# Kernel tuning notes

Measured on AMD Instinct MI355X. Metric: run time of the kernel, lower is better.

Reference implementation:

```python
import jax, jax.numpy as jnp
import numpy as np

# ---- static configuration matching init_kwargs ----
SEG = 2                 # segment_size hard-coded in the module
MUL0, MUL1 = 256, 128   # irreps = 256x0e + 128x1o
G = MUL1 // SEG         # 64 groups of 2x1o
INV_DIM = MUL0 + 3 * G  # 448 scalars (0e) after concat with channel_mix
N_IRREPS = INV_DIM + MUL1 + G + 3 * G  # 832 total irreps after regroup
N_NODES = 32768
EPS = 1e-6
_ISQ2 = 1.0 / np.sqrt(2.0)
_ISQ3 = 1.0 / np.sqrt(3.0)
_ISQ6 = 1.0 / np.sqrt(6.0)


def _cg_l2(a, b):
    """CG contraction 1 x 1 -> 2: project a_i b_j onto the 5 orthonormal
    symmetric-traceless basis matrices. a, b: [..., 3] -> [..., 5]."""
    ax, ay, az = a[..., 0], a[..., 1], a[..., 2]
    bx, by, bz = b[..., 0], b[..., 1], b[..., 2]
    return jnp.stack([
        (ax * by + ay * bx) * _ISQ2,
        (ax * bz + az * bx) * _ISQ2,
        (ay * bz + az * by) * _ISQ2,
        (ax * bx - ay * by) * _ISQ2,
        (2 * az * bz - ax * bx - ay * by) * _ISQ6,
    ], axis=-1)


def setup_inputs() -> dict:
    key = jax.random.key(0)
    k = jax.random.split(key, 5)
    return {
        "x":   jax.random.normal(k[0], (N_NODES, MUL0 + 3 * MUL1), dtype=jnp.float32),
        "W1":  jax.random.normal(k[1], (INV_DIM, INV_DIM),   dtype=jnp.float32),
        "W2":  jax.random.normal(k[2], (INV_DIM, N_IRREPS),  dtype=jnp.float32),
        "Wl0": jax.random.normal(k[3], (INV_DIM, MUL0),      dtype=jnp.float32),
        "Wl1": jax.random.normal(k[4], (MUL1, MUL1),         dtype=jnp.float32),
    }


def reference(x, W1, W2, Wl0, Wl1):
    N = x.shape[0]
    dt = x.dtype
    s = x[:, :MUL0]                       # [N, 256]  0e features
    v = x[:, MUL0:].reshape(N, MUL1, 3)   # [N, 128, 3]  1o features

    # ---- segmented tensor_square: groups of 2x1o -> 3x0e + 1x1e + 3x2e ----
    vg = v.reshape(N, G, SEG, 3)
    a, b = vg[:, :, 0], vg[:, :, 1]
    sq2 = jnp.sqrt(jnp.asarray(2.0, dt))
    # 0e: symmetric pairs (0,0), (0,1)*sqrt2, (1,1); CG = delta_ij/sqrt3
    t0 = jnp.stack([(a * a).sum(-1), sq2 * (a * b).sum(-1), (b * b).sum(-1)], -1) * _ISQ3  # [N,G,3]
    # 1e: antisymmetric pair (0,1); CG = eps/sqrt2, pair factor sqrt2 -> plain cross
    t1 = jnp.cross(a, b)                                                                   # [N,G,3]
    # 2e: symmetric pairs
    t2 = jnp.stack([_cg_l2(a, a), sq2 * _cg_l2(a, b), _cg_l2(b, b)], 2)                    # [N,G,3,5]

    # ---- concatenate + regroup (axis_to_mul folds group axis into mul) ----
    s_all = jnp.concatenate([s, t0.reshape(N, 3 * G)], -1)  # [N,448]  448x0e
    v1o = v                                                 # [N,128,3] 128x1o
    v1e = t1                                                # [N,64,3]   64x1e
    v2e = t2.reshape(N, 3 * G, 5)                           # [N,192,5] 192x2e

    # ---- gating MLP on invariants: [448 -> 448 (silu) -> 832] ----
    inv_fan = jnp.sqrt(jnp.asarray(INV_DIM, dt))
    h = jax.nn.silu(s_all @ W1 / inv_fan)
    gates = h @ W2 / inv_fan                                # [N, 832] one scalar per irrep
    g0, g1o, g1e, g2e = jnp.split(gates, [INV_DIM, INV_DIM + MUL1, INV_DIM + MUL1 + G], -1)
    s_all = s_all * g0
    v1o = v1o * g1o[..., None]
    # (v1e * g1e, v2e * g2e are dropped by the Linear below -> omitted, output identical)
    del v1e, v2e, g1e, g2e

    # ---- e3nn Linear to output irreps 256x0e + 128x1o (1e, 2e have no output) ----
    o0 = s_all @ Wl0 / inv_fan                                                   # [N,256]
    o1 = jnp.einsum('nmi,mk->nki', v1o, Wl1) / jnp.sqrt(jnp.asarray(MUL1, dt))   # [N,128,3]

    # ---- equivariant layer norm ----
    mu = o0.mean(-1, keepdims=True)
    var = ((o0 - mu) ** 2).mean(-1, keepdims=True)
    o0 = (o0 - mu) * jax.lax.rsqrt(var + EPS)
    rms = jnp.sqrt((o1 ** 2).mean((-2, -1), keepdims=True) + EPS)
    o1 = o1 / rms

    return jnp.concatenate([o0, o1.reshape(N, 3 * MUL1)], -1)  # [N, 640]
```

## Files before the change

kernel.cpp:

```cpp
#include <hip/hip_runtime.h>
#include <math.h>


typedef float floatx4 __attribute__((ext_vector_type(4)));
typedef __bf16 bf16x8 __attribute__((ext_vector_type(8)));

__device__ __forceinline__ unsigned short f2bf(float f) {
    union { float f; unsigned u; } v; v.f = f;
    unsigned r = v.u + 0x7FFFu + ((v.u >> 16) & 1u);
    return (unsigned short)(r >> 16);
}
__device__ __forceinline__ float bf2f(unsigned short u) {
    union { unsigned u; float f; } v; v.u = ((unsigned)u) << 16; return v.f;
}

__global__ __launch_bounds__(256) void wcast_kernel(
    const float* __restrict__ W1, const float* __restrict__ W2,
    const float* __restrict__ Wl0, const float* __restrict__ Wl1,
    unsigned short* __restrict__ W1T, unsigned short* __restrict__ W2T,
    unsigned short* __restrict__ Wl0T, unsigned short* __restrict__ Wl1T)
{
    int idx = blockIdx.x * 256 + threadIdx.x;
    if (idx < 200704) {
        int j = idx / 448, k = idx - j * 448;
        W1T[idx] = f2bf(W1[k * 448 + j]);
    } else if (idx < 200704 + 258048) {
        int r = idx - 200704;
        int j = r / 448, k = r - j * 448;
        W2T[r] = f2bf(W2[k * 832 + j]);
    } else if (idx < 200704 + 258048 + 114688) {
        int r = idx - (200704 + 258048);
        int j = r / 448, k = r - j * 448;
        Wl0T[r] = f2bf(Wl0[k * 256 + j]);
    } else if (idx < 200704 + 258048 + 114688 + 16384) {
        int r = idx - (200704 + 258048 + 114688);
        int j = r / 128, m = r - j * 128;
        Wl1T[r] = f2bf(Wl1[m * 128 + j]);
    }
}

template<int MT, int NT>
__device__ __forceinline__ void gemm_ktiles(
    const unsigned short* __restrict__ Bt, const int ldb, const int kTot, const int colBase,
    const unsigned short* __restrict__ Albs, const int ldsA, const int rowBase,
    unsigned short* __restrict__ Bs,
    const int tid, const int l15, const int quad, const int wn,
    floatx4 (&acc)[MT][NT])
{
    constexpr int NU = NT * 256;
    for (int k0 = 0; k0 < kTot; k0 += 32) {
        __syncthreads();
        #pragma unroll
        for (int u0 = 0; u0 < NU; u0 += 512) {
            int u = u0 + tid;
            if (u0 + 512 <= NU || u < NU) {
                int col = u >> 2, part = u & 3;
                *(uint4*)&Bs[col * 40 + part * 8] =
                    *(const uint4*)(Bt + (colBase + col) * ldb + k0 + part * 8);
            }
        }
        __syncthreads();
        bf16x8 af[MT];
        #pragma unroll
        for (int mt = 0; mt < MT; ++mt)
            af[mt] = *(const bf16x8*)&Albs[(rowBase + mt * 16 + l15) * ldsA + k0 + quad * 8];
        #pragma unroll
        for (int j = 0; j < NT; ++j) {
            bf16x8 bfv = *(const bf16x8*)&Bs[((wn + 4 * j) * 16 + l15) * 40 + quad * 8];
            #pragma unroll
            for (int mt = 0; mt < MT; ++mt)
                acc[mt][j] = __builtin_amdgcn_mfma_f32_16x16x32_bf16(af[mt], bfv, acc[mt][j], 0, 0, 0);
        }
    }
}

__global__ __launch_bounds__(512, 2) void fused_kernel(
    const float* __restrict__ x,
    const unsigned short* __restrict__ W1T,
    const unsigned short* __restrict__ W2T,
    const unsigned short* __restrict__ Wl0T,
    const unsigned short* __restrict__ Wl1T,
    float* __restrict__ out)
{
    __shared__ unsigned short sa[64][472];
    __shared__ unsigned short hb[64][472];
    __shared__ unsigned short BsG1[17920];
    __shared__ float red[832];

    const int tid  = threadIdx.x;
    const int lane = tid & 63;
    const int l15  = lane & 15;
    const int quad = lane >> 4;
    const int w    = tid >> 6;
    const int wm   = w >> 2;
    const int wn   = w & 3;
    const int n0   = blockIdx.x * 64;

    const float s1 = 0.047245559f;
    const float s2 = 0.088388348f;

    {
        const int r = tid >> 3, sub = tid & 7;
        const float* xr = x + (size_t)(n0 + r) * 640;
        #pragma unroll
        for (int i = 0; i < 8; ++i) {
            int c4 = i * 8 + sub;
            float4 f = *(const float4*)(xr + c4 * 4);
            uint2 p;
            p.x = (unsigned)f2bf(f.x) | ((unsigned)f2bf(f.y) << 16);
            p.y = (unsigned)f2bf(f.z) | ((unsigned)f2bf(f.w) << 16);
            *(uint2*)&sa[r][c4 * 4] = p;
        }
        const float* xv = xr + 256;
        #pragma unroll
        for (int i = 0; i < 8; ++i) {
            int g = i * 8 + sub;
            const float2* vg = (const float2*)(xv + 6 * g);
            float2 p0 = vg[0], p1 = vg[1], p2 = vg[2];
            float ax = p0.x, ay = p0.y, az = p1.x;
            float bx = p1.y, by = p2.x, bz = p2.y;
            float aa = ax*ax + ay*ay + az*az;
            float ab = ax*bx + ay*by + az*bz;
            float bb = bx*bx + by*by + bz*bz;
            const float ISQ3 = 0.57735026918962576f;
            const float SQ2  = 1.41421356237309505f;
            sa[r][256 + 3*g]     = f2bf(aa * ISQ3);
            sa[r][256 + 3*g + 1] = f2bf(SQ2 * ab * ISQ3);
            sa[r][256 + 3*g + 2] = f2bf(bb * ISQ3);
        }
    }

    {
        floatx4 acc[2][7] = {};
        gemm_ktiles<2,7>(W1T, 448, 448, 0, &sa[0][0], 472, wm*32, BsG1, tid, l15, quad, wn, acc);
        #pragma unroll
        for (int j = 0; j < 7; ++j) {
            const int col = (wn + 4*j) * 16 + l15;
            #pragma unroll
            for (int mt = 0; mt < 2; ++mt)
                #pragma unroll
                for (int r = 0; r < 4; ++r) {
                    float v = acc[mt][j][r] * s1;
                    v = v / (1.f + __expf(-v));
                    hb[wm*32 + mt*16 + quad*4 + r][col] = f2bf(v);
                }
        }
    }

    {
        floatx4 acc1[2][5] = {};
        floatx4 acc2[2][4] = {};
        gemm_ktiles<2,5>(W2T, 448, 448, 0,   &hb[0][0], 472, wm*32, BsG1, tid, l15, quad, wn, acc1);
        gemm_ktiles<2,4>(W2T, 448, 448, 320, &hb[0][0], 472, wm*32, BsG1, tid, l15, quad, wn, acc2);
        __syncthreads();
        unsigned short* g1p = BsG1;
        #pragma unroll
        for (int j = 0; j < 5; ++j) {
            const int col = (wn + 4*j) * 16 + l15;
            #pragma unroll
            for (int mt = 0; mt < 2; ++mt)
                #pragma unroll
                for (int r = 0; r < 4; ++r) {
                    const int row = wm*32 + mt*16 + quad*4 + r;
                    hb[row][col] = f2bf(bf2f(sa[row][col]) * (acc1[mt][j][r] * s1));
                }
        }
        #pragma unroll
        for (int j = 0; j < 4; ++j) {
            const int colb = 320 + (wn + 4*j) * 16;
            if (colb < 448) {
                const int col = colb + l15;
                #pragma unroll
                for (int mt = 0; mt < 2; ++mt)
                    #pragma unroll
                    for (int r = 0; r < 4; ++r) {
                        const int row = wm*32 + mt*16 + quad*4 + r;
                        hb[row][col] = f2bf(bf2f(sa[row][col]) * (acc2[mt][j][r] * s1));
                    }
            } else {
                const int m = colb - 448 + l15;
                #pragma unroll
                for (int mt = 0; mt < 2; ++mt)
                    #pragma unroll
                    for (int r = 0; r < 4; ++r) {
                        const int row = wm*32 + mt*16 + quad*4 + r;
                        g1p[row * 128 + m] = f2bf(acc2[mt][j][r] * s1);
                    }
            }
        }
        __syncthreads();
    }

    {
        unsigned short* wmp = &sa[0][0];
        const unsigned short* g1p = BsG1;
        #pragma unroll
        for (int e0 = 0; e0 < 6144; e0 += 512) {
            int e4 = e0 + tid;
            int rl = e4 / 96;
            int c4 = (e4 - rl * 96) * 4;
            float4 xv = *(const float4*)(x + (size_t)(n0 + rl) * 640 + 256 + c4);
            float vv[4] = {xv.x, xv.y, xv.z, xv.w};
            #pragma unroll
            for (int d = 0; d < 4; ++d) {
                int rem = c4 + d;
                int m = rem / 3;
                int i = rem - 3 * m;
                wmp[(rl * 3 + i) * 136 + m] = f2bf(vv[d] * bf2f(g1p[rl * 128 + m]));
            }
        }
        __syncthreads();
    }

    {
        floatx4 acc[2][4] = {};
        gemm_ktiles<2,4>(Wl0T, 448, 448, 0, &hb[0][0], 472, wm*32, BsG1, tid, l15, quad, wn, acc);
        #pragma unroll
        for (int mt = 0; mt < 2; ++mt)
            #pragma unroll
            for (int r = 0; r < 4; ++r) {
                float sv = 0.f, sq = 0.f;
                #pragma unroll
                for (int j = 0; j < 4; ++j) {
                    float v = acc[mt][j][r] * s1;
                    sv += v; sq += v * v;
                }
                #pragma unroll
                for (int off = 1; off <= 8; off <<= 1) {
                    sv += __shfl_xor(sv, off);
                    sq += __shfl_xor(sq, off);
                }
                if (l15 == 0) {
                    const int row = wm*32 + mt*16 + quad*4 + r;
                    red[row * 8 + wn * 2]     = sv;
                    red[row * 8 + wn * 2 + 1] = sq;
                }
            }
        __syncthreads();
        #pragma unroll
        for (int mt = 0; mt < 2; ++mt)
            #pragma unroll
            for (int r = 0; r < 4; ++r) {
                const int row = wm*32 + mt*16 + quad*4 + r;
                float ts = red[row*8+0] + red[row*8+2] + red[row*8+4] + red[row*8+6];
                float tq = red[row*8+1] + red[row*8+3] + red[row*8+5] + red[row*8+7];
                float mu  = ts * (1.f/256.f);
                float var = tq * (1.f/256.f) - mu * mu;
                float rln = rsqrtf(var + 1e-6f);
                float* orow = out + (size_t)(n0 + row) * 640;
                #pragma unroll
                for (int j = 0; j < 4; ++j)
                    orow[(wn + 4*j)*16 + l15] = (acc[mt][j][r] * s1 - mu) * rln;
            }
    }

    {
        floatx4 acc[6][2] = {};
        gemm_ktiles<6,2>(Wl1T, 128, 128, 0, &sa[0][0] , 136, wm*96, BsG1, tid, l15, quad, wn, acc);
        #pragma unroll
        for (int mt = 0; mt < 6; ++mt)
            #pragma unroll
            for (int r = 0; r < 4; ++r) {
                float q = 0.f;
                #pragma unroll
                for (int j = 0; j < 2; ++j) {
                    float v = acc[mt][j][r] * s2;
                    q += v * v;
                }
                #pragma unroll
                for (int off = 1; off <= 8; off <<= 1) q += __shfl_xor(q, off);
                if (l15 == 0) {
                    const int row = wm*96 + mt*16 + quad*4 + r;
                    red[row * 4 + wn] = q;
                }
            }
        __syncthreads();
        if (tid < 64) {
            float s = 0.f;
            #pragma unroll
            for (int rr = 0; rr < 3; ++rr)
                #pragma unroll
                for (int w2 = 0; w2 < 4; ++w2)
                    s += red[(tid*3 + rr) * 4 + w2];
            red[768 + tid] = rsqrtf(s * (1.f/384.f) + 1e-6f);
        }
        __syncthreads();
        #pragma unroll
        for (int mt = 0; mt < 6; ++mt)
            #pragma unroll
            for (int r = 0; r < 4; ++r) {
                const int row = wm*96 + mt*16 + quad*4 + r;
                const int nl  = row / 3;
                const int i   = row - 3 * nl;
                const float rms = red[768 + nl];
                float* op = out + (size_t)(n0 + nl) * 640 + 256 + i;
                #pragma unroll
                for (int j = 0; j < 2; ++j)
                    op[3 * ((wn + 4*j)*16 + l15)] = acc[mt][j][r] * s2 * rms;
            }
    }
}

extern "C" void kernel_launch(void* const* d_in, const int* in_sizes, int n_in,
                              void* d_out, int out_size, void* d_ws, size_t ws_size,
                              hipStream_t stream) {
    const float* x   = (const float*)d_in[0];
    const float* W1  = (const float*)d_in[1];
    const float* W2  = (const float*)d_in[2];
    const float* Wl0 = (const float*)d_in[3];
    const float* Wl1 = (const float*)d_in[4];
    float* out = (float*)d_out;
    char* ws = (char*)d_ws;

    unsigned short* W1T  = (unsigned short*)(ws + 0);
    unsigned short* W2T  = (unsigned short*)(ws + 401408);
    unsigned short* Wl0T = (unsigned short*)(ws + 917504);
    unsigned short* Wl1T = (unsigned short*)(ws + 1146880);

    wcast_kernel<<<dim3(2304), dim3(256), 0, stream>>>(W1, W2, Wl0, Wl1, W1T, W2T, Wl0T, Wl1T);
    fused_kernel<<<dim3(512), dim3(512), 0, stream>>>(x, W1T, W2T, Wl0T, Wl1T, out);
}
```

Baseline: 283.2 us.

## Pre-swizzle weights into MFMA fragment order and stream B directly from global

The weight-cast kernel now writes each weight matrix in a layout where every lane's 8-element bf16 B fragment is contiguous per 16-column tile and 32-wide k-chunk. The GEMM loop then loads B fragments straight from global/L2 into registers, with no LDS staging and no per-k-tile __syncthreads. The two W2 GEMM passes are merged into one with 9 column tiles, and explicit barriers are added between stages. This removes LDS traffic and barrier stalls, at the cost of relying on L2 and cache latency for every B load, with no explicit prefetch.

```diff
diff --git a/kernel.cpp b/kernel.cpp
--- a/kernel.cpp
+++ b/kernel.cpp
@@ -17,56 +17,60 @@
 __global__ __launch_bounds__(256) void wcast_kernel(
     const float* __restrict__ W1, const float* __restrict__ W2,
     const float* __restrict__ Wl0, const float* __restrict__ Wl1,
-    unsigned short* __restrict__ W1T, unsigned short* __restrict__ W2T,
-    unsigned short* __restrict__ Wl0T, unsigned short* __restrict__ Wl1T)
+    unsigned short* __restrict__ W1F, unsigned short* __restrict__ W2F,
+    unsigned short* __restrict__ Wl0F, unsigned short* __restrict__ Wl1F)
 {
     int idx = blockIdx.x * 256 + threadIdx.x;
     if (idx < 200704) {
-        int j = idx / 448, k = idx - j * 448;
-        W1T[idx] = f2bf(W1[k * 448 + j]);
-    } else if (idx < 200704 + 258048) {
+        int e = idx & 7, lane = (idx >> 3) & 63, r2 = idx >> 9;
+        int kc = r2 % 14, t = r2 / 14;
+        int col = t * 16 + (lane & 15);
+        int k   = kc * 32 + (lane >> 4) * 8 + e;
+        W1F[idx] = f2bf(W1[k * 448 + col]);
+    } else if (idx < 458752) {
         int r = idx - 200704;
-        int j = r / 448, k = r - j * 448;
-        W2T[r] = f2bf(W2[k * 832 + j]);
-    } else if (idx < 200704 + 258048 + 114688) {
-        int r = idx - (200704 + 258048);
-        int j = r / 448, k = r - j * 448;
-        Wl0T[r] = f2bf(Wl0[k * 256 + j]);
-    } else if (idx < 200704 + 258048 + 114688 + 16384) {
-        int r = idx - (200704 + 258048 + 114688);
-        int j = r / 128, m = r - j * 128;
-        Wl1T[r] = f2bf(Wl1[m * 128 + j]);
-    }
-}
-
-template<int MT, int NT>
-__device__ __forceinline__ void gemm_ktiles(
-    const unsigned short* __restrict__ Bt, const int ldb, const int kTot, const int colBase,
+        int e = r & 7, lane = (r >> 3) & 63, r2 = r >> 9;
+        int kc = r2 % 14, t = r2 / 14;
+        int col = t * 16 + (lane & 15);
+        int k   = kc * 32 + (lane >> 4) * 8 + e;
+        W2F[r] = f2bf(W2[k * 832 + col]);
+    } else if (idx < 573440) {
+        int r = idx - 458752;
+        int e = r & 7, lane = (r >> 3) & 63, r2 = r >> 9;
+        int kc = r2 % 14, t = r2 / 14;
+        int col = t * 16 + (lane & 15);
+        int k   = kc * 32 + (lane >> 4) * 8 + e;
+        Wl0F[r] = f2bf(Wl0[k * 256 + col]);
+    } else if (idx < 589824) {
+        int r = idx - 573440;
+        int e = r & 7, lane = (r >> 3) & 63, r2 = r >> 9;
+        int kc = r2 % 4, t = r2 / 4;
+        int col = t * 16 + (lane & 15);
+        int k   = kc * 32 + (lane >> 4) * 8 + e;
+        Wl1F[r] = f2bf(Wl1[k * 128 + col]);
+    }
+}
+
+template<int MT, int NT, int NKC>
+__device__ __forceinline__ void gemm_stream(
+    const unsigned short* __restrict__ BF, const int tileBase,
     const unsigned short* __restrict__ Albs, const int ldsA, const int rowBase,
-    unsigned short* __restrict__ Bs,
-    const int tid, const int l15, const int quad, const int wn,
+    const int lane, const int l15, const int quad, const int wn,
     floatx4 (&acc)[MT][NT])
 {
-    constexpr int NU = NT * 256;
-    for (int k0 = 0; k0 < kTot; k0 += 32) {
-        __syncthreads();
-        #pragma unroll
-        for (int u0 = 0; u0 < NU; u0 += 512) {
-            int u = u0 + tid;
-            if (u0 + 512 <= NU || u < NU) {
-                int col = u >> 2, part = u & 3;
-                *(uint4*)&Bs[col * 40 + part * 8] =
-                    *(const uint4*)(Bt + (colBase + col) * ldb + k0 + part * 8);
-            }
-        }
-        __syncthreads();
+    const unsigned short* bp[NT];
+    #pragma unroll
+    for (int j = 0; j < NT; ++j)
+        bp[j] = BF + ((size_t)(tileBase + wn + 4 * j) * NKC * 64 + lane) * 8;
+    #pragma unroll
+    for (int kc = 0; kc < NKC; ++kc) {
         bf16x8 af[MT];
         #pragma unroll
         for (int mt = 0; mt < MT; ++mt)
-            af[mt] = *(const bf16x8*)&Albs[(rowBase + mt * 16 + l15) * ldsA + k0 + quad * 8];
+            af[mt] = *(const bf16x8*)&Albs[(rowBase + mt * 16 + l15) * ldsA + kc * 32 + quad * 8];
         #pragma unroll
         for (int j = 0; j < NT; ++j) {
-            bf16x8 bfv = *(const bf16x8*)&Bs[((wn + 4 * j) * 16 + l15) * 40 + quad * 8];
+            bf16x8 bfv = *(const bf16x8*)(bp[j] + kc * 512);
             #pragma unroll
             for (int mt = 0; mt < MT; ++mt)
                 acc[mt][j] = __builtin_amdgcn_mfma_f32_16x16x32_bf16(af[mt], bfv, acc[mt][j], 0, 0, 0);
@@ -76,15 +80,15 @@
 
 __global__ __launch_bounds__(512, 2) void fused_kernel(
     const float* __restrict__ x,
-    const unsigned short* __restrict__ W1T,
-    const unsigned short* __restrict__ W2T,
-    const unsigned short* __restrict__ Wl0T,
-    const unsigned short* __restrict__ Wl1T,
+    const unsigned short* __restrict__ W1F,
+    const unsigned short* __restrict__ W2F,
+    const unsigned short* __restrict__ Wl0F,
+    const unsigned short* __restrict__ Wl1F,
     float* __restrict__ out)
 {
     __shared__ unsigned short sa[64][472];
     __shared__ unsigned short hb[64][472];
-    __shared__ unsigned short BsG1[17920];
+    __shared__ unsigned short g1[64][128];
     __shared__ float red[832];
 
     const int tid  = threadIdx.x;
@@ -129,10 +133,11 @@
             sa[r][256 + 3*g + 2] = f2bf(bb * ISQ3);
         }
     }
+    __syncthreads();
 
     {
         floatx4 acc[2][7] = {};
-        gemm_ktiles<2,7>(W1T, 448, 448, 0, &sa[0][0], 472, wm*32, BsG1, tid, l15, quad, wn, acc);
+        gemm_stream<2,7,14>(W1F, 0, &sa[0][0], 472, wm*32, lane, l15, quad, wn, acc);
         #pragma unroll
         for (int j = 0; j < 7; ++j) {
             const int col = (wn + 4*j) * 16 + l15;
@@ -146,28 +151,15 @@
                 }
         }
     }
-
-    {
-        floatx4 acc1[2][5] = {};
-        floatx4 acc2[2][4] = {};
-        gemm_ktiles<2,5>(W2T, 448, 448, 0,   &hb[0][0], 472, wm*32, BsG1, tid, l15, quad, wn, acc1);
-        gemm_ktiles<2,4>(W2T, 448, 448, 320, &hb[0][0], 472, wm*32, BsG1, tid, l15, quad, wn, acc2);
+    __syncthreads();
+
+    {
+        floatx4 acc[2][9] = {};
+        gemm_stream<2,9,14>(W2F, 0, &hb[0][0], 472, wm*32, lane, l15, quad, wn, acc);
         __syncthreads();
-        unsigned short* g1p = BsG1;
-        #pragma unroll
-        for (int j = 0; j < 5; ++j) {
-            const int col = (wn + 4*j) * 16 + l15;
-            #pragma unroll
-            for (int mt = 0; mt < 2; ++mt)
-                #pragma unroll
-                for (int r = 0; r < 4; ++r) {
-                    const int row = wm*32 + mt*16 + quad*4 + r;
-                    hb[row][col] = f2bf(bf2f(sa[row][col]) * (acc1[mt][j][r] * s1));
-                }
-        }
-        #pragma unroll
-        for (int j = 0; j < 4; ++j) {
-            const int colb = 320 + (wn + 4*j) * 16;
+        #pragma unroll
+        for (int j = 0; j < 9; ++j) {
+            const int colb = (wn + 4*j) * 16;
             if (colb < 448) {
                 const int col = colb + l15;
                 #pragma unroll
@@ -175,7 +167,7 @@
                     #pragma unroll
                     for (int r = 0; r < 4; ++r) {
                         const int row = wm*32 + mt*16 + quad*4 + r;
-                        hb[row][col] = f2bf(bf2f(sa[row][col]) * (acc2[mt][j][r] * s1));
+                        hb[row][col] = f2bf(bf2f(sa[row][col]) * (acc[mt][j][r] * s1));
                     }
             } else {
                 const int m = colb - 448 + l15;
@@ -184,16 +176,15 @@
                     #pragma unroll
                     for (int r = 0; r < 4; ++r) {
                         const int row = wm*32 + mt*16 + quad*4 + r;
-                        g1p[row * 128 + m] = f2bf(acc2[mt][j][r] * s1);
+                        g1[row][m] = f2bf(acc[mt][j][r] * s1);
                     }
             }
         }
-        __syncthreads();
-    }
+    }
+    __syncthreads();
 
     {
         unsigned short* wmp = &sa[0][0];
-        const unsigned short* g1p = BsG1;
         #pragma unroll
         for (int e0 = 0; e0 < 6144; e0 += 512) {
             int e4 = e0 + tid;
@@ -206,15 +197,15 @@
                 int rem = c4 + d;
                 int m = rem / 3;
                 int i = rem - 3 * m;
-                wmp[(rl * 3 + i) * 136 + m] = f2bf(vv[d] * bf2f(g1p[rl * 128 + m]));
-            }
-        }
-        __syncthreads();
-    }
+                wmp[(rl * 3 + i) * 136 + m] = f2bf(vv[d] * bf2f(g1[rl][m]));
+            }
+        }
+    }
+    __syncthreads();
 
     {
         floatx4 acc[2][4] = {};
-        gemm_ktiles<2,4>(Wl0T, 448, 448, 0, &hb[0][0], 472, wm*32, BsG1, tid, l15, quad, wn, acc);
+        gemm_stream<2,4,14>(Wl0F, 0, &hb[0][0], 472, wm*32, lane, l15, quad, wn, acc);
         #pragma unroll
         for (int mt = 0; mt < 2; ++mt)
             #pragma unroll
@@ -253,10 +244,11 @@
                     orow[(wn + 4*j)*16 + l15] = (acc[mt][j][r] * s1 - mu) * rln;
             }
     }
+    __syncthreads();
 
     {
         floatx4 acc[6][2] = {};
-        gemm_ktiles<6,2>(Wl1T, 128, 128, 0, &sa[0][0] , 136, wm*96, BsG1, tid, l15, quad, wn, acc);
+        gemm_stream<6,2,4>(Wl1F, 0, &sa[0][0] , 136, wm*96, lane, l15, quad, wn, acc);
         #pragma unroll
         for (int mt = 0; mt < 6; ++mt)
             #pragma unroll
@@ -312,11 +304,11 @@
     float* out = (float*)d_out;
     char* ws = (char*)d_ws;
 
-    unsigned short* W1T  = (unsigned short*)(ws + 0);
-    unsigned short* W2T  = (unsigned short*)(ws + 401408);
-    unsigned short* Wl0T = (unsigned short*)(ws + 917504);
-    unsigned short* Wl1T = (unsigned short*)(ws + 1146880);
-
-    wcast_kernel<<<dim3(2304), dim3(256), 0, stream>>>(W1, W2, Wl0, Wl1, W1T, W2T, Wl0T, Wl1T);
-    fused_kernel<<<dim3(512), dim3(512), 0, stream>>>(x, W1T, W2T, Wl0T, Wl1T, out);
-}
+    unsigned short* W1F  = (unsigned short*)(ws + 0);
+    unsigned short* W2F  = (unsigned short*)(ws + 401408);
+    unsigned short* Wl0F = (unsigned short*)(ws + 917504);
+    unsigned short* Wl1F = (unsigned short*)(ws + 1146880);
+
+    wcast_kernel<<<dim3(2304), dim3(256), 0, stream>>>(W1, W2, Wl0, Wl1, W1F, W2F, Wl0F, Wl1F);
+    fused_kernel<<<dim3(512), dim3(512), 0, stream>>>(x, W1F, W2F, Wl0F, Wl1F, out);
+}
```

After: 259.4 us. -8.4%, faster.
